# Performance work log

Measured on AMD Instinct MI355X. Metric: run time of the kernel, lower is better.

The kernel has to match this reference:

```python
import jax, jax.numpy as jnp
import numpy as np

B, N, F, U, E = 4, 10000, 128, 128, 160000


def setup_inputs() -> dict:
    key = jax.random.key(0)
    ks = jax.random.split(key, 5)
    s = lambda d: 1.0 / np.sqrt(d)
    return {
        "node_features": jax.random.normal(ks[0], (B, N, F), dtype=jnp.float32),
        "edge_indices": jax.random.randint(ks[1], (E, 2), 0, N, dtype=jnp.int64),
        "W_t": jax.random.normal(ks[2], (F, U), dtype=jnp.float32) * s(F),
        "b_t": jnp.zeros((U,), jnp.float32),
        "W_a": jax.random.normal(ks[3], (2 * U, 1), dtype=jnp.float32) * s(2 * U),
        "b_a": jnp.zeros((1,), jnp.float32),
        "W_c": jax.random.normal(ks[4], (2 * U, U), dtype=jnp.float32) * s(2 * U),
        "b_c": jnp.zeros((U,), jnp.float32),
    }


def reference(node_features, edge_indices, W_t, b_t, W_a, b_a, W_c, b_c):
    b, n, _ = node_features.shape
    e = edge_indices.shape[0]
    u = W_t.shape[1]
    # transform: Dense + relu  [B,N,U]
    h = jax.nn.relu(jnp.einsum('bnf,fu->bnu', node_features, W_t) + b_t)
    src = edge_indices[:, 0]
    tgt = edge_indices[:, 1]
    source_nodes = h[:, src, :]   # [B,E,U]
    target_nodes = h[:, tgt, :]   # [B,E,U]
    edge_features = jnp.concatenate([source_nodes, target_nodes], axis=-1)  # [B,E,2U]
    att = jnp.tanh(jnp.einsum('beu,uo->beo', edge_features, W_a) + b_a)     # [B,E,1]
    # original softmax is over axis=0 of the flattened [B*E,1] tensor
    attn = jax.nn.softmax(att.reshape(-1, 1), axis=0).reshape(b, e, 1)
    weighted = attn * target_nodes  # [B,E,U]
    # scatter-add messages onto source nodes, per batch element
    scattered = jax.vmap(lambda m: jax.ops.segment_sum(m, src, num_segments=n))(weighted)  # [B,N,U]
    out = jax.nn.relu(
        jnp.einsum('bnu,uo->bno', jnp.concatenate([h, scattered], axis=-1), W_c) + b_c
    )
    return out
```

## Files before the change

### kernel.cpp

```cpp
#include <hip/hip_runtime.h>

#define BB 4
#define NN 10000
#define FF 128
#define UU 128
#define EE 160000

typedef __bf16 bf16x8 __attribute__((ext_vector_type(8)));
typedef float  f32x4  __attribute__((ext_vector_type(4)));

#define WS_S      0
#define WS_DEG    256
#define WS_OFFS   40448
#define WS_CUR    80640
#define WS_TGT    120832
#define WS_EXW    760832
#define WS_P      3320832
#define WS_Q      3480832
#define WS_BTG    3640832
#define WS_BCG    3673600
#define WS_HS     3739136

__global__ __launch_bounds__(256) void k_prep(const float* __restrict__ Wt,
                                              const float* __restrict__ Wc,
                                              char* __restrict__ ws) {
  const int gid = blockIdx.x * 256 + threadIdx.x;
  uint4* zp = (uint4*)ws;
  uint4 z = {0u, 0u, 0u, 0u};
  for (int i = gid; i < 2528; i += 2048) zp[i] = z;

  __bf16* Btg = (__bf16*)(ws + WS_BTG);
  __bf16* Bcg = (__bf16*)(ws + WS_BCG);
  {
    int i = gid;
    int n = i & 127, kb8 = i >> 7;
    int kc = kb8 >> 2, kbq = kb8 & 3;
    int lane = (n & 15) | (kbq << 4), c = n >> 4;
    const float* src = Wt + (size_t)kb8 * 8 * 128 + n;
    bf16x8 v;
#pragma unroll
    for (int j = 0; j < 8; ++j) v[j] = (__bf16)src[(size_t)j * 128];
    *(bf16x8*)(Btg + ((kc * 8 + c) * 512 + lane * 8)) = v;
  }
#pragma unroll
  for (int it = 0; it < 2; ++it) {
    int i = gid + it * 2048;
    int n = i & 127, kb8 = i >> 7;
    int kc = kb8 >> 2, kbq = kb8 & 3;
    int lane = (n & 15) | (kbq << 4), c = n >> 4;
    const float* src = Wc + (size_t)kb8 * 8 * 128 + n;
    bf16x8 v;
#pragma unroll
    for (int j = 0; j < 8; ++j) v[j] = (__bf16)src[(size_t)j * 128];
    *(bf16x8*)(Bcg + ((kc * 8 + c) * 512 + lane * 8)) = v;
  }
}

__global__ __launch_bounds__(512) void k_gemm_h(
    const float* __restrict__ nf, const __bf16* __restrict__ Btg,
    const float* __restrict__ bt, const float* __restrict__ Wa,
    const int* __restrict__ eidx, int* __restrict__ deg,
    __bf16* __restrict__ hs, float* __restrict__ p2, float* __restrict__ q2) {
  {
    int e = blockIdx.x * 512 + threadIdx.x;
    if (e < EE) atomicAdd(&deg[eidx[2 * e]], 1);
  }
  __shared__ __bf16 Bt[32 * 512];
  const int tid = threadIdx.x;
  {
    uint4* d = (uint4*)Bt;
    const uint4* s = (const uint4*)Btg;
#pragma unroll
    for (int i = tid; i < 2048; i += 512) d[i] = s[i];
  }
  __syncthreads();

  const int wid = tid >> 6, lane = tid & 63;
  const int lr = lane & 15, lg = lane >> 4;
  const int row0 = blockIdx.x * 128 + wid * 16;

  f32x4 acc[8];
#pragma unroll
  for (int c = 0; c < 8; ++c)
#pragma unroll
    for (int r = 0; r < 4; ++r) acc[c][r] = 0.f;

  const int arow = min(row0 + lr, 39999);

#pragma unroll
  for (int k0 = 0; k0 < 128; k0 += 32) {
    int kk = k0 + lg * 8;
    const float4* ap = (const float4*)(nf + (size_t)arow * 128 + kk);
    float4 a0 = ap[0], a1 = ap[1];
    bf16x8 af;
    af[0] = (__bf16)a0.x; af[1] = (__bf16)a0.y; af[2] = (__bf16)a0.z; af[3] = (__bf16)a0.w;
    af[4] = (__bf16)a1.x; af[5] = (__bf16)a1.y; af[6] = (__bf16)a1.z; af[7] = (__bf16)a1.w;
#pragma unroll
    for (int c = 0; c < 8; ++c) {
      bf16x8 bf = *(const bf16x8*)(Bt + (((k0 >> 5) << 3) + c) * 512 + lane * 8);
      acc[c] = __builtin_amdgcn_mfma_f32_16x16x32_bf16(af, bf, acc[c], 0, 0, 0);
    }
  }

#pragma unroll
  for (int r = 0; r < 4; ++r) {
    int row = row0 + lg * 4 + r;
    bool ok = row < 40000;
    int b = row / NN;
    int n = row - b * NN;
    size_t dst = ((size_t)n * 4 + b) * 256;
    float pr = 0.f, qr = 0.f;
#pragma unroll
    for (int c = 0; c < 8; ++c) {
      int col = c * 16 + lr;
      float v = acc[c][r] + bt[col];
      v = fmaxf(v, 0.f);
      if (ok) hs[dst + col] = (__bf16)v;
      pr += v * Wa[col];
      qr += v * Wa[128 + col];
    }
#pragma unroll
    for (int m = 1; m < 16; m <<= 1) {
      pr += __shfl_xor(pr, m);
      qr += __shfl_xor(qr, m);
    }
    if (lr == 0 && ok) {
      p2[n * 4 + b] = pr;
      q2[n * 4 + b] = qr;
    }
  }
}

__global__ __launch_bounds__(1024) void k_scan(const int* __restrict__ deg,
                                               int* __restrict__ offs,
                                               int* __restrict__ cursor) {
  const int t = threadIdx.x, lane = t & 63, wv = t >> 6;
  const int base = t * 10;
  int local[10];
  int s = 0;
#pragma unroll
  for (int i = 0; i < 10; ++i) {
    int v = (base + i < NN) ? deg[base + i] : 0;
    local[i] = s;
    s += v;
  }
  const int tsum = s;
#pragma unroll
  for (int off = 1; off < 64; off <<= 1) {
    int v = __shfl_up(s, off);
    if (lane >= off) s += v;
  }
  __shared__ int wsum[16];
  if (lane == 63) wsum[wv] = s;
  __syncthreads();
  int add = 0;
#pragma unroll
  for (int w = 0; w < 16; ++w) {
    int v = wsum[w];
    if (w < wv) add += v;
  }
  int pre = add + s - tsum;
#pragma unroll
  for (int i = 0; i < 10; ++i) {
    int idx = base + i;
    if (idx < NN) {
      int o = pre + local[i];
      offs[idx] = o;
      cursor[idx] = o;
    }
  }
  if (t == 1023) offs[NN] = pre + tsum;
}

__global__ __launch_bounds__(256) void k_att(const int* __restrict__ eidx,
                                             const float4* __restrict__ p2,
                                             const float4* __restrict__ q2,
                                             const float* __restrict__ ba,
                                             int* __restrict__ cursor,
                                             int* __restrict__ tgts,
                                             float* __restrict__ exwT,
                                             float* __restrict__ S) {
  int e = blockIdx.x * 256 + threadIdx.x;
  int s = eidx[2 * e], t = eidx[2 * e + 1];
  float4 pv = p2[s];
  float4 qv = q2[t];
  float bias = ba[0];
#define ATT(pc, qc, out)                              \
  {                                                   \
    float a = (pc) + (qc) + bias;                     \
    float z = __expf(2.f * a);                        \
    float th = 1.f - __fdividef(2.f, z + 1.f);        \
    (out) = __expf(th);                               \
  }
  float v0, v1, v2, v3;
  ATT(pv.x, qv.x, v0)
  ATT(pv.y, qv.y, v1)
  ATT(pv.z, qv.z, v2)
  ATT(pv.w, qv.w, v3)
#undef ATT
  int pos = atomicAdd(&cursor[s], 1);
  tgts[pos] = t;
  exwT[pos] = v0;
  exwT[EE + pos] = v1;
  exwT[2 * EE + pos] = v2;
  exwT[3 * EE + pos] = v3;
  float vs = v0 + v1 + v2 + v3;
#pragma unroll
  for (int m = 1; m < 64; m <<= 1) vs += __shfl_xor(vs, m);
  __shared__ float part[4];
  int wid = threadIdx.x >> 6, lane = threadIdx.x & 63;
  if (lane == 0) part[wid] = vs;
  __syncthreads();
  if (threadIdx.x == 0) atomicAdd(S, part[0] + part[1] + part[2] + part[3]);
}

__global__ __launch_bounds__(256) void k_agg(
    const int* __restrict__ tgts, const int* __restrict__ offs,
    const float* __restrict__ exwT, const float* __restrict__ S,
    __bf16* __restrict__ hs) {
  const int wid = threadIdx.x >> 6, lane = threadIdx.x & 63;
  const int n = blockIdx.x * 4 + wid;
  const int myb = lane >> 4, sub = lane & 15;
  const int o0 = offs[n], o1 = offs[n + 1];
  const uint4* __restrict__ hu4 = (const uint4*)hs;
  float acc[8];
#pragma unroll
  for (int i = 0; i < 8; ++i) acc[i] = 0.f;

  const int lbase = myb * 32 + sub;
  const int wsrc = myb << 4;
  for (int base = o0; base < o1; base += 16) {
    int idx = base + sub;
    bool valid = idx < o1;
    int t_l = valid ? tgts[idx] : 0;
    float w_l = valid ? exwT[(size_t)myb * EE + idx] : 0.f;
    int cnt = min(16, o1 - base);
    for (int j = 0; j < cnt; j += 4) {
      int t0 = __shfl(t_l, j + 0);
      int t1 = __shfl(t_l, j + 1);
      int t2 = __shfl(t_l, j + 2);
      int t3 = __shfl(t_l, j + 3);
      float m0 = __shfl(w_l, wsrc | (j + 0));
      float m1 = __shfl(w_l, wsrc | (j + 1));
      float m2 = __shfl(w_l, wsrc | (j + 2));
      float m3 = __shfl(w_l, wsrc | (j + 3));
      uint4 va = hu4[(size_t)t0 * 128 + lbase];
      uint4 vb = hu4[(size_t)t1 * 128 + lbase];
      uint4 vc = hu4[(size_t)t2 * 128 + lbase];
      uint4 vd = hu4[(size_t)t3 * 128 + lbase];
#define LO(x) __uint_as_float((x) << 16)
#define HI(x) __uint_as_float((x)&0xffff0000u)
#define ACC(m, v)                                                   \
  acc[0] = fmaf((m), LO((v).x), acc[0]);                            \
  acc[1] = fmaf((m), HI((v).x), acc[1]);                            \
  acc[2] = fmaf((m), LO((v).y), acc[2]);                            \
  acc[3] = fmaf((m), HI((v).y), acc[3]);                            \
  acc[4] = fmaf((m), LO((v).z), acc[4]);                            \
  acc[5] = fmaf((m), HI((v).z), acc[5]);                            \
  acc[6] = fmaf((m), LO((v).w), acc[6]);                            \
  acc[7] = fmaf((m), HI((v).w), acc[7]);
      ACC(m0, va)
      ACC(m1, vb)
      ACC(m2, vc)
      ACC(m3, vd)
#undef ACC
#undef LO
#undef HI
    }
  }
  const float invS = 1.0f / S[0];
  uint4 st;
  unsigned* sp = (unsigned*)&st;
#pragma unroll
  for (int i = 0; i < 4; ++i) {
    unsigned ux = __float_as_uint(acc[2 * i] * invS);
    ux = (ux + 0x7fffu + ((ux >> 16) & 1u)) >> 16;
    unsigned uy = __float_as_uint(acc[2 * i + 1] * invS);
    uy = (uy + 0x7fffu + ((uy >> 16) & 1u)) >> 16;
    sp[i] = ux | (uy << 16);
  }
  ((uint4*)hs)[(size_t)n * 128 + myb * 32 + 16 + sub] = st;
}

__global__ __launch_bounds__(512) void k_gemm_out(
    const __bf16* __restrict__ hs, const __bf16* __restrict__ Bcg,
    const float* __restrict__ bc, float* __restrict__ out) {
  __shared__ __bf16 Bt[64 * 512];
  const int tid = threadIdx.x;
  {
    uint4* d = (uint4*)Bt;
    const uint4* s = (const uint4*)Bcg;
#pragma unroll
    for (int i = tid; i < 4096; i += 512) d[i] = s[i];
  }
  __syncthreads();

  const int wid = tid >> 6, lane = tid & 63;
  const int lr = lane & 15, lg = lane >> 4;
  const int row0 = blockIdx.x * 128 + wid * 16;

  f32x4 acc[8];
#pragma unroll
  for (int c = 0; c < 8; ++c)
#pragma unroll
    for (int r = 0; r < 4; ++r) acc[c][r] = 0.f;

  const int arow = min(row0 + lr, 39999);

#pragma unroll
  for (int k0 = 0; k0 < 256; k0 += 32) {
    int kk = k0 + lg * 8;
    bf16x8 af = *(const bf16x8*)(hs + (size_t)arow * 256 + kk);
#pragma unroll
    for (int c = 0; c < 8; ++c) {
      bf16x8 bf = *(const bf16x8*)(Bt + (((k0 >> 5) << 3) + c) * 512 + lane * 8);
      acc[c] = __builtin_amdgcn_mfma_f32_16x16x32_bf16(af, bf, acc[c], 0, 0, 0);
    }
  }

#pragma unroll
  for (int r = 0; r < 4; ++r) {
    int m = row0 + lg * 4 + r;
    if (m < 40000) {
      int n = m >> 2, b = m & 3;
      size_t orow = ((size_t)b * NN + n) * 128;
#pragma unroll
      for (int c = 0; c < 8; ++c) {
        int col = c * 16 + lr;
        float v = acc[c][r] + bc[col];
        out[orow + col] = fmaxf(v, 0.f);
      }
    }
  }
}

extern "C" void kernel_launch(void* const* d_in, const int* in_sizes, int n_in,
                              void* d_out, int out_size, void* d_ws,
                              size_t ws_size, hipStream_t stream) {
  const float* nf = (const float*)d_in[0];
  const int* eidx = (const int*)d_in[1];
  const float* Wt = (const float*)d_in[2];
  const float* bt = (const float*)d_in[3];
  const float* Wa = (const float*)d_in[4];
  const float* ba = (const float*)d_in[5];
  const float* Wc = (const float*)d_in[6];
  const float* bc = (const float*)d_in[7];
  float* out = (float*)d_out;

  char* w = (char*)d_ws;
  float* S = (float*)(w + WS_S);
  int* deg = (int*)(w + WS_DEG);
  int* offs = (int*)(w + WS_OFFS);
  int* cursor = (int*)(w + WS_CUR);
  int* tgts = (int*)(w + WS_TGT);
  float* exwT = (float*)(w + WS_EXW);
  float* p2 = (float*)(w + WS_P);
  float* q2 = (float*)(w + WS_Q);
  __bf16* Btg = (__bf16*)(w + WS_BTG);
  __bf16* Bcg = (__bf16*)(w + WS_BCG);
  __bf16* hs = (__bf16*)(w + WS_HS);

  k_prep<<<8, 256, 0, stream>>>(Wt, Wc, w);
  k_gemm_h<<<313, 512, 0, stream>>>(nf, Btg, bt, Wa, eidx, deg, hs, p2, q2);
  k_scan<<<1, 1024, 0, stream>>>(deg, offs, cursor);
  k_att<<<625, 256, 0, stream>>>(eidx, (const float4*)p2, (const float4*)q2,
                                 ba, cursor, tgts, exwT, S);
  k_agg<<<2500, 256, 0, stream>>>(tgts, offs, exwT, S, hs);
  k_gemm_out<<<313, 512, 0, stream>>>(hs, Bcg, bc, out);
}
```

Baseline: 160.7 us.

## Gather neighbor features from an fp8 copy of h in aggregation

The transform GEMM now also writes an fp8 (e4m3) copy of h in a lane-packed column order, and the aggregation kernel gathers from it instead of the bf16 copy, halving gathered bytes. Wc's second-half rows are permuted in prep so the permuted scattered columns line up. Edge weights are stored interleaved as float4 per edge instead of batch-transposed, so each edge needs one load. The cost is lower precision in the aggregated messages, plus an extra write of the fp8 buffer.

Result: faster. 153.8 us, median of 2 (-4.3%).

```diff
diff --git a/kernel.cpp b/kernel.cpp
--- a/kernel.cpp
+++ b/kernel.cpp
@@ -8,6 +8,7 @@
 
 typedef __bf16 bf16x8 __attribute__((ext_vector_type(8)));
 typedef float  f32x4  __attribute__((ext_vector_type(4)));
+typedef float  f32x2  __attribute__((ext_vector_type(2)));
 
 #define WS_S      0
 #define WS_DEG    256
@@ -20,6 +21,7 @@
 #define WS_BTG    3640832
 #define WS_BCG    3673600
 #define WS_HS     3739136
+#define WS_H8     24219136
 
 __global__ __launch_bounds__(256) void k_prep(const float* __restrict__ Wt,
                                               const float* __restrict__ Wc,
@@ -48,10 +50,17 @@
     int n = i & 127, kb8 = i >> 7;
     int kc = kb8 >> 2, kbq = kb8 & 3;
     int lane = (n & 15) | (kbq << 4), c = n >> 4;
-    const float* src = Wc + (size_t)kb8 * 8 * 128 + n;
     bf16x8 v;
-#pragma unroll
-    for (int j = 0; j < 8; ++j) v[j] = (__bf16)src[(size_t)j * 128];
+    if (kb8 < 16) {
+      const float* src = Wc + (size_t)kb8 * 8 * 128 + n;
+#pragma unroll
+      for (int j = 0; j < 8; ++j) v[j] = (__bf16)src[(size_t)j * 128];
+    } else {
+      int sub = kb8 - 16;
+      const float* src = Wc + (size_t)(128 + sub) * 128 + n;
+#pragma unroll
+      for (int j = 0; j < 8; ++j) v[j] = (__bf16)src[(size_t)j * 16 * 128];
+    }
     *(bf16x8*)(Bcg + ((kc * 8 + c) * 512 + lane * 8)) = v;
   }
 }
@@ -60,7 +69,8 @@
     const float* __restrict__ nf, const __bf16* __restrict__ Btg,
     const float* __restrict__ bt, const float* __restrict__ Wa,
     const int* __restrict__ eidx, int* __restrict__ deg,
-    __bf16* __restrict__ hs, float* __restrict__ p2, float* __restrict__ q2) {
+    __bf16* __restrict__ hs, char* __restrict__ h8,
+    float* __restrict__ p2, float* __restrict__ q2) {
   {
     int e = blockIdx.x * 512 + threadIdx.x;
     if (e < EE) atomicAdd(&deg[eidx[2 * e]], 1);
@@ -109,15 +119,25 @@
     int b = row / NN;
     int n = row - b * NN;
     size_t dst = ((size_t)n * 4 + b) * 256;
+    float vv[8];
     float pr = 0.f, qr = 0.f;
 #pragma unroll
     for (int c = 0; c < 8; ++c) {
       int col = c * 16 + lr;
       float v = acc[c][r] + bt[col];
       v = fmaxf(v, 0.f);
+      vv[c] = v;
       if (ok) hs[dst + col] = (__bf16)v;
       pr += v * Wa[col];
       qr += v * Wa[128 + col];
+    }
+    int d0 = __builtin_amdgcn_cvt_pk_fp8_f32(vv[0], vv[1], 0, false);
+    d0 = __builtin_amdgcn_cvt_pk_fp8_f32(vv[2], vv[3], d0, true);
+    int d1 = __builtin_amdgcn_cvt_pk_fp8_f32(vv[4], vv[5], 0, false);
+    d1 = __builtin_amdgcn_cvt_pk_fp8_f32(vv[6], vv[7], d1, true);
+    if (ok) {
+      uint2 st = make_uint2((unsigned)d0, (unsigned)d1);
+      *(uint2*)(h8 + ((size_t)n * 4 + b) * 128 + lr * 8) = st;
     }
 #pragma unroll
     for (int m = 1; m < 16; m <<= 1) {
@@ -178,7 +198,7 @@
                                              const float* __restrict__ ba,
                                              int* __restrict__ cursor,
                                              int* __restrict__ tgts,
-                                             float* __restrict__ exwT,
+                                             float4* __restrict__ exw,
                                              float* __restrict__ S) {
   int e = blockIdx.x * 256 + threadIdx.x;
   int s = eidx[2 * e], t = eidx[2 * e + 1];
@@ -200,10 +220,7 @@
 #undef ATT
   int pos = atomicAdd(&cursor[s], 1);
   tgts[pos] = t;
-  exwT[pos] = v0;
-  exwT[EE + pos] = v1;
-  exwT[2 * EE + pos] = v2;
-  exwT[3 * EE + pos] = v3;
+  exw[pos] = make_float4(v0, v1, v2, v3);
   float vs = v0 + v1 + v2 + v3;
 #pragma unroll
   for (int m = 1; m < 64; m <<= 1) vs += __shfl_xor(vs, m);
@@ -216,24 +233,25 @@
 
 __global__ __launch_bounds__(256) void k_agg(
     const int* __restrict__ tgts, const int* __restrict__ offs,
-    const float* __restrict__ exwT, const float* __restrict__ S,
-    __bf16* __restrict__ hs) {
+    const float4* __restrict__ exw, const float* __restrict__ S,
+    const char* __restrict__ h8, __bf16* __restrict__ hs) {
   const int wid = threadIdx.x >> 6, lane = threadIdx.x & 63;
   const int n = blockIdx.x * 4 + wid;
   const int myb = lane >> 4, sub = lane & 15;
   const int o0 = offs[n], o1 = offs[n + 1];
-  const uint4* __restrict__ hu4 = (const uint4*)hs;
+  const uint2* __restrict__ h8u = (const uint2*)h8;
   float acc[8];
 #pragma unroll
   for (int i = 0; i < 8; ++i) acc[i] = 0.f;
 
-  const int lbase = myb * 32 + sub;
+  const int lslot = myb * 16 + sub;
   const int wsrc = myb << 4;
   for (int base = o0; base < o1; base += 16) {
     int idx = base + sub;
     bool valid = idx < o1;
     int t_l = valid ? tgts[idx] : 0;
-    float w_l = valid ? exwT[(size_t)myb * EE + idx] : 0.f;
+    float4 w4 = valid ? exw[idx] : make_float4(0.f, 0.f, 0.f, 0.f);
+    float w_l = (myb == 0) ? w4.x : (myb == 1) ? w4.y : (myb == 2) ? w4.z : w4.w;
     int cnt = min(16, o1 - base);
     for (int j = 0; j < cnt; j += 4) {
       int t0 = __shfl(t_l, j + 0);
@@ -244,28 +262,26 @@
       float m1 = __shfl(w_l, wsrc | (j + 1));
       float m2 = __shfl(w_l, wsrc | (j + 2));
       float m3 = __shfl(w_l, wsrc | (j + 3));
-      uint4 va = hu4[(size_t)t0 * 128 + lbase];
-      uint4 vb = hu4[(size_t)t1 * 128 + lbase];
-      uint4 vc = hu4[(size_t)t2 * 128 + lbase];
-      uint4 vd = hu4[(size_t)t3 * 128 + lbase];
-#define LO(x) __uint_as_float((x) << 16)
-#define HI(x) __uint_as_float((x)&0xffff0000u)
-#define ACC(m, v)                                                   \
-  acc[0] = fmaf((m), LO((v).x), acc[0]);                            \
-  acc[1] = fmaf((m), HI((v).x), acc[1]);                            \
-  acc[2] = fmaf((m), LO((v).y), acc[2]);                            \
-  acc[3] = fmaf((m), HI((v).y), acc[3]);                            \
-  acc[4] = fmaf((m), LO((v).z), acc[4]);                            \
-  acc[5] = fmaf((m), HI((v).z), acc[5]);                            \
-  acc[6] = fmaf((m), LO((v).w), acc[6]);                            \
-  acc[7] = fmaf((m), HI((v).w), acc[7]);
-      ACC(m0, va)
-      ACC(m1, vb)
-      ACC(m2, vc)
-      ACC(m3, vd)
-#undef ACC
-#undef LO
-#undef HI
+      uint2 va = h8u[(size_t)t0 * 64 + lslot];
+      uint2 vb = h8u[(size_t)t1 * 64 + lslot];
+      uint2 vc = h8u[(size_t)t2 * 64 + lslot];
+      uint2 vd = h8u[(size_t)t3 * 64 + lslot];
+#define ACC8(m, v)                                                        \
+  {                                                                       \
+    f32x2 f01 = __builtin_amdgcn_cvt_pk_f32_fp8((int)(v).x, false);       \
+    f32x2 f23 = __builtin_amdgcn_cvt_pk_f32_fp8((int)(v).x, true);        \
+    f32x2 f45 = __builtin_amdgcn_cvt_pk_f32_fp8((int)(v).y, false);       \
+    f32x2 f67 = __builtin_amdgcn_cvt_pk_f32_fp8((int)(v).y, true);        \
+    acc[0] = fmaf((m), f01.x, acc[0]); acc[1] = fmaf((m), f01.y, acc[1]); \
+    acc[2] = fmaf((m), f23.x, acc[2]); acc[3] = fmaf((m), f23.y, acc[3]); \
+    acc[4] = fmaf((m), f45.x, acc[4]); acc[5] = fmaf((m), f45.y, acc[5]); \
+    acc[6] = fmaf((m), f67.x, acc[6]); acc[7] = fmaf((m), f67.y, acc[7]); \
+  }
+      ACC8(m0, va)
+      ACC8(m1, vb)
+      ACC8(m2, vc)
+      ACC8(m3, vd)
+#undef ACC8
     }
   }
   const float invS = 1.0f / S[0];
@@ -353,18 +369,19 @@
   int* offs = (int*)(w + WS_OFFS);
   int* cursor = (int*)(w + WS_CUR);
   int* tgts = (int*)(w + WS_TGT);
-  float* exwT = (float*)(w + WS_EXW);
+  float4* exw = (float4*)(w + WS_EXW);
   float* p2 = (float*)(w + WS_P);
   float* q2 = (float*)(w + WS_Q);
   __bf16* Btg = (__bf16*)(w + WS_BTG);
   __bf16* Bcg = (__bf16*)(w + WS_BCG);
   __bf16* hs = (__bf16*)(w + WS_HS);
+  char* h8 = w + WS_H8;
 
   k_prep<<<8, 256, 0, stream>>>(Wt, Wc, w);
-  k_gemm_h<<<313, 512, 0, stream>>>(nf, Btg, bt, Wa, eidx, deg, hs, p2, q2);
+  k_gemm_h<<<313, 512, 0, stream>>>(nf, Btg, bt, Wa, eidx, deg, hs, h8, p2, q2);
   k_scan<<<1, 1024, 0, stream>>>(deg, offs, cursor);
   k_att<<<625, 256, 0, stream>>>(eidx, (const float4*)p2, (const float4*)q2,
-                                 ba, cursor, tgts, exwT, S);
-  k_agg<<<2500, 256, 0, stream>>>(tgts, offs, exwT, S, hs);
+                                 ba, cursor, tgts, exw, S);
+  k_agg<<<2500, 256, 0, stream>>>(tgts, offs, exw, S, h8, hs);
   k_gemm_out<<<313, 512, 0, stream>>>(hs, Bcg, bc, out);
 }
```
